# Optimization experiments

Hardware: AMD Instinct MI355X
Metric: run time of the kernel (lower is better)

Reference implementation:

```python
import jax, jax.numpy as jnp
import numpy as np

S, B, E, H, D, P = 4096, 8, 1024, 16, 64, 64


def setup_inputs() -> dict:
    key = jax.random.key(0)
    ks = jax.random.split(key, 6)
    scale = 1.0 / np.sqrt(E)
    return {
        "x": jax.random.normal(ks[0], (S, B, E), dtype=jnp.float32),
        "w_qkv": jax.random.normal(ks[1], (3 * E, E), dtype=jnp.float32) * scale,
        "w_out": jax.random.normal(ks[2], (E, E), dtype=jnp.float32) * scale,
        "b_out": jax.random.normal(ks[3], (E,), dtype=jnp.float32) * 0.01,
        "w_f": jax.random.normal(ks[4], (P, D), dtype=jnp.float32) * (1.0 / np.sqrt(D)),
        "b_f": jax.random.normal(ks[5], (P,), dtype=jnp.float32) * 0.01,
    }


def reference(x, w_qkv, w_out, b_out, w_f, b_f):
    # x: (S, B, E). qkv_proj has no bias.
    qkv = jnp.einsum("sbe,fe->sbf", x, w_qkv)  # (S, B, 3E)
    q, k, v = jnp.split(qkv, 3, axis=-1)

    def to_heads(t):
        # view (S,B,H,D) then transpose(0,2) -> (H,B,S,D)
        return t.reshape(S, B, H, D).transpose(2, 1, 0, 3)

    q, k, v = to_heads(q), to_heads(k), to_heads(v)

    # feature map: Linear(D->P) + ReLU, applied to q and k
    q_p = jax.nn.relu(jnp.einsum("hbsd,pd->hbsp", q, w_f) + b_f)
    k_p = jax.nn.relu(jnp.einsum("hbsd,pd->hbsp", k, w_f) + b_f)

    # linear attention: O(n) via k'^T v then q' @ (k'^T v)
    kv = jnp.einsum("hbsp,hbsd->hbpd", k_p, v)          # (H,B,P,D)
    num = jnp.einsum("hbsp,hbpd->hbsd", q_p, kv)         # (H,B,S,D)
    k_sum = k_p.sum(axis=-2)                              # (H,B,P)
    normalizer = jnp.einsum("hbsp,hbp->hbs", q_p, k_sum)[..., None]  # (H,B,S,1)
    attn = num / (normalizer + 1e-8)

    # back to (S, B, E)
    out = attn.transpose(2, 1, 0, 3).reshape(S, B, E)
    return jnp.einsum("sbe,fe->sbf", out, w_out) + b_out
```

## Files before the change

### kernel.cpp

```cpp
#include <hip/hip_runtime.h>
#include <hip/hip_bf16.h>
#include <stdint.h>

#define S_LEN 4096
#define B_DIM 8
#define E_DIM 1024
#define H_DIM 16
#define M_ROWS (S_LEN * B_DIM)
#define N_QKV (3 * E_DIM)
#define HB_DIM (H_DIM * B_DIM)

typedef float f32x4 __attribute__((ext_vector_type(4)));
typedef short bf16x8 __attribute__((ext_vector_type(8)));

#define MFMA16(a, b, c) __builtin_amdgcn_mfma_f32_16x16x32_bf16(a, b, c, 0, 0, 0)

__device__ __forceinline__ short f2bf(float f) {
  __hip_bfloat16 h = __float2bfloat16(f);
  short s;
  __builtin_memcpy(&s, &h, 2);
  return s;
}
__device__ __forceinline__ float bf2f(short b) {
  unsigned u = ((unsigned)(unsigned short)b) << 16;
  float f;
  __builtin_memcpy(&f, &u, 4);
  return f;
}
__device__ __forceinline__ void gl_lds16(const void* g, void* l) {
  __builtin_amdgcn_global_load_lds(
      (const __attribute__((address_space(1))) void*)g,
      (__attribute__((address_space(3))) void*)l, 16, 0, 0);
}

__global__ __launch_bounds__(256) void cast_all(
    const float* __restrict__ x, const float* __restrict__ wqkv,
    const float* __restrict__ wout, const float* __restrict__ wf,
    short* __restrict__ xb, short* __restrict__ wqb,
    short* __restrict__ wob, short* __restrict__ wfb) {
  const long n_x = (long)M_ROWS * E_DIM;
  const long n_wq = 3L * E_DIM * E_DIM;
  const long n_wo = (long)E_DIM * E_DIM;
  long idx = ((long)blockIdx.x * 256 + threadIdx.x) * 4;
  const float* src;
  short* dst;
  if (idx < n_x) {
    src = x + idx; dst = xb + idx;
  } else if ((idx -= n_x) < n_wq) {
    src = wqkv + idx; dst = wqb + idx;
  } else if ((idx -= n_wq) < n_wo) {
    src = wout + idx; dst = wob + idx;
  } else {
    idx -= n_wo;
    src = wf + idx; dst = wfb + idx;
  }
  float4 v = *(const float4*)src;
  short4 o;
  o.x = f2bf(v.x); o.y = f2bf(v.y); o.z = f2bf(v.z); o.w = f2bf(v.w);
  *(short4*)dst = o;
}

template <int OUT_F32>
__global__ __launch_bounds__(512, 2) void gemm256(
    const short* __restrict__ A, const short* __restrict__ Bm,
    void* __restrict__ Cout, const float* __restrict__ bias, int N, int K) {
  __shared__ short As[4 * 8192];
  __shared__ short Bs[4 * 8192];
  const int t = threadIdx.x;
  const int w = t >> 6, l = t & 63;
  const int q = l >> 4, c = l & 15;
  const int wm = w >> 2, wn = w & 3;

  const int nwg = gridDim.x;
  const int cpx = nwg >> 3;
  const int lid = ((int)blockIdx.x & 7) * cpx + ((int)blockIdx.x >> 3);
  const int bm = (lid & 127) << 8;
  const int bn = (lid >> 7) << 8;

  const long Kb = (long)K * 2;
  const int srow = t >> 2;
  const int scolb = (((t & 3) ^ ((t >> 3) & 3)) << 4);
  const char* gA = (const char*)A + (long)(bm + srow) * Kb + scolb;
  const char* gB = (const char*)Bm + (long)(bn + srow) * Kb + scolb;
  const long chb = 128 * Kb;
  char* lA = (char*)As + (w << 10);
  char* lB = (char*)Bs + (w << 10);

  const int qs = q ^ ((c >> 1) & 3);
  const short* ar = As + ((wm << 7) + c) * 32 + (qs << 3);
  const short* br = Bs + ((wn << 6) + c) * 32 + (qs << 3);

  f32x4 acc[8][4];
#pragma unroll
  for (int i = 0; i < 8; i++)
#pragma unroll
    for (int j = 0; j < 4; j++) acc[i][j] = (f32x4){0.f, 0.f, 0.f, 0.f};

#pragma unroll
  for (int p = 0; p < 3; p++) {
    const char* sa = gA + (long)p * 64;
    const char* sb = gB + (long)p * 64;
    char* da = lA + p * 16384;
    char* db = lB + p * 16384;
    gl_lds16(sa, da);
    gl_lds16(sa + chb, da + 8192);
    gl_lds16(sb, db);
    gl_lds16(sb + chb, db + 8192);
  }
  asm volatile("s_waitcnt vmcnt(8)\n\ts_barrier" ::: "memory");

  const int NT = K >> 5;
  for (int tt = 0; tt < NT; ++tt) {
    const int slot = (tt & 3) * 8192;
    const int pslot = ((tt + 3) & 3) * 16384;
    const int pkt = (tt + 3 < NT) ? tt + 3 : NT - 1;
    const short* ap = ar + slot;
    const short* bp = br + slot;
    const char* sa = gA + (long)pkt * 64;
    const char* sb = gB + (long)pkt * 64;

    bf16x8 af[8], bfr[4];
#pragma unroll
    for (int mi = 0; mi < 4; mi++) af[mi] = *(const bf16x8*)(ap + mi * 512);
#pragma unroll
    for (int ni = 0; ni < 4; ni++) bfr[ni] = *(const bf16x8*)(bp + ni * 512);
    gl_lds16(sa, lA + pslot);
    gl_lds16(sa + chb, lA + pslot + 8192);
    __builtin_amdgcn_s_barrier();
    __builtin_amdgcn_s_setprio(1);
#pragma unroll
    for (int mi = 0; mi < 4; mi++)
#pragma unroll
      for (int ni = 0; ni < 4; ni++)
        acc[mi][ni] = MFMA16(af[mi], bfr[ni], acc[mi][ni]);
    __builtin_amdgcn_s_setprio(0);
    __builtin_amdgcn_s_barrier();
#pragma unroll
    for (int mi = 4; mi < 8; mi++) af[mi] = *(const bf16x8*)(ap + mi * 512);
    gl_lds16(sb, lB + pslot);
    gl_lds16(sb + chb, lB + pslot + 8192);
    __builtin_amdgcn_s_barrier();
    __builtin_amdgcn_s_setprio(1);
#pragma unroll
    for (int mi = 4; mi < 8; mi++)
#pragma unroll
      for (int ni = 0; ni < 4; ni++)
        acc[mi][ni] = MFMA16(af[mi], bfr[ni], acc[mi][ni]);
    __builtin_amdgcn_s_setprio(0);
    asm volatile("s_waitcnt vmcnt(8)\n\ts_barrier" ::: "memory");
  }
  asm volatile("s_waitcnt vmcnt(0)" ::: "memory");

  if (OUT_F32) {
    float* C = (float*)Cout;
#pragma unroll
    for (int ni = 0; ni < 4; ni++) {
      int n = bn + (wn << 6) + ni * 16 + c;
      float bo = bias[n];
#pragma unroll
      for (int mi = 0; mi < 8; mi++)
#pragma unroll
        for (int r = 0; r < 4; r++) {
          int m = bm + (wm << 7) + mi * 16 + (q << 2) + r;
          C[(long)m * N + n] = acc[mi][ni][r] + bo;
        }
    }
  } else {
    short* C = (short*)Cout;
#pragma unroll
    for (int ni = 0; ni < 4; ni++) {
      int n = bn + (wn << 6) + ni * 16 + c;
#pragma unroll
      for (int mi = 0; mi < 8; mi++)
#pragma unroll
        for (int r = 0; r < 4; r++) {
          int m = bm + (wm << 7) + mi * 16 + (q << 2) + r;
          C[(long)m * N + n] = f2bf(acc[mi][ni][r]);
        }
    }
  }
}

__global__ __launch_bounds__(256) void feature_kernel(
    const short* __restrict__ qkv, const short* __restrict__ wfb,
    const float* __restrict__ b_f, short* __restrict__ Qp,
    short* __restrict__ KpT, short* __restrict__ VT) {
  const int bx = blockIdx.x;
  const int sblk = bx & 15, b = (bx >> 4) & 7, h = bx >> 7;
  const int t = threadIdx.x, w = t >> 6, l = t & 63;
  const int q = l >> 4, c = l & 15;
  const int s_base = sblk * 256 + w * 64;
  const int hb = h * 8 + b;

  bf16x8 wf[4][2];
#pragma unroll
  for (int ti = 0; ti < 4; ti++)
#pragma unroll
    for (int kk = 0; kk < 2; kk++)
      wf[ti][kk] = *(const bf16x8*)(wfb + (ti * 16 + c) * 64 + kk * 32 + q * 8);

  float bfc[4];
#pragma unroll
  for (int ni = 0; ni < 4; ni++) bfc[ni] = b_f[ni * 16 + c];

  f32x4 acc[4][4];
  bf16x8 xf[4][2];

#pragma unroll
  for (int i = 0; i < 4; i++)
#pragma unroll
    for (int j = 0; j < 4; j++) acc[i][j] = (f32x4){0.f, 0.f, 0.f, 0.f};
#pragma unroll
  for (int mi = 0; mi < 4; mi++) {
    long ridx = (long)((s_base + mi * 16 + c) * 8 + b) * N_QKV;
#pragma unroll
    for (int kk = 0; kk < 2; kk++)
      xf[mi][kk] = *(const bf16x8*)(qkv + ridx + h * 64 + kk * 32 + q * 8);
  }
#pragma unroll
  for (int kk = 0; kk < 2; kk++)
#pragma unroll
    for (int mi = 0; mi < 4; mi++)
#pragma unroll
      for (int ni = 0; ni < 4; ni++)
        acc[mi][ni] = MFMA16(xf[mi][kk], wf[ni][kk], acc[mi][ni]);
#pragma unroll
  for (int mi = 0; mi < 4; mi++)
#pragma unroll
    for (int ni = 0; ni < 4; ni++)
#pragma unroll
      for (int r = 0; r < 4; r++) {
        int s = s_base + mi * 16 + q * 4 + r;
        float v = acc[mi][ni][r] + bfc[ni];
        v = fmaxf(v, 0.f);
        Qp[((long)hb * S_LEN + s) * 64 + ni * 16 + c] = f2bf(v);
      }

#pragma unroll
  for (int i = 0; i < 4; i++)
#pragma unroll
    for (int j = 0; j < 4; j++) acc[i][j] = (f32x4){0.f, 0.f, 0.f, 0.f};
#pragma unroll
  for (int si = 0; si < 4; si++) {
    long ridx = (long)((s_base + si * 16 + c) * 8 + b) * N_QKV;
#pragma unroll
    for (int kk = 0; kk < 2; kk++)
      xf[si][kk] =
          *(const bf16x8*)(qkv + ridx + E_DIM + h * 64 + kk * 32 + q * 8);
  }
#pragma unroll
  for (int kk = 0; kk < 2; kk++)
#pragma unroll
    for (int pi = 0; pi < 4; pi++)
#pragma unroll
      for (int si = 0; si < 4; si++)
        acc[pi][si] = MFMA16(wf[pi][kk], xf[si][kk], acc[pi][si]);
#pragma unroll
  for (int pi = 0; pi < 4; pi++)
#pragma unroll
    for (int r = 0; r < 4; r++) {
      int p = pi * 16 + q * 4 + r;
      float bb = b_f[p];
#pragma unroll
      for (int si = 0; si < 4; si++) {
        int s = s_base + si * 16 + c;
        float v = acc[pi][si][r] + bb;
        v = fmaxf(v, 0.f);
        KpT[((long)hb * 64 + p) * S_LEN + s] = f2bf(v);
      }
    }

  bf16x8 id0 = {0, 0, 0, 0, 0, 0, 0, 0}, id1 = {0, 0, 0, 0, 0, 0, 0, 0};
#pragma unroll
  for (int j = 0; j < 8; j++) {
    int k = q * 8 + j;
    id0[j] = (short)((k == c) ? 0x3F80 : 0);
    id1[j] = (short)((k == c + 16) ? 0x3F80 : 0);
  }
#pragma unroll
  for (int i = 0; i < 4; i++)
#pragma unroll
    for (int j = 0; j < 4; j++) acc[i][j] = (f32x4){0.f, 0.f, 0.f, 0.f};
#pragma unroll
  for (int si = 0; si < 4; si++) {
    long ridx = (long)((s_base + si * 16 + c) * 8 + b) * N_QKV;
#pragma unroll
    for (int kc = 0; kc < 2; kc++)
      xf[si][kc] =
          *(const bf16x8*)(qkv + ridx + 2 * E_DIM + h * 64 + kc * 32 + q * 8);
  }
#pragma unroll
  for (int kc = 0; kc < 2; kc++)
#pragma unroll
    for (int si = 0; si < 4; si++) {
      acc[kc * 2 + 0][si] = MFMA16(id0, xf[si][kc], acc[kc * 2 + 0][si]);
      acc[kc * 2 + 1][si] = MFMA16(id1, xf[si][kc], acc[kc * 2 + 1][si]);
    }
#pragma unroll
  for (int dt = 0; dt < 4; dt++)
#pragma unroll
    for (int si = 0; si < 4; si++)
#pragma unroll
      for (int r = 0; r < 4; r++) {
        int d = (dt >> 1) * 32 + (dt & 1) * 16 + q * 4 + r;
        int s = s_base + si * 16 + c;
        VT[((long)hb * 64 + d) * S_LEN + s] = f2bf(acc[dt][si][r]);
      }
}

__global__ __launch_bounds__(256) void kv_kernel(const short* __restrict__ KpT,
                                                 const short* __restrict__ VT,
                                                 float* __restrict__ kvf) {
  const int hb = blockIdx.y, sc = blockIdx.x;
  const int t = threadIdx.x, w = t >> 6, l = t & 63;
  const int q = l >> 4, c = l & 15;
  const int s0 = sc * 512 + w * 128;
  const short* vb = VT + (long)hb * 64 * S_LEN;
  const short* kb = KpT + (long)hb * 64 * S_LEN;

  f32x4 acc[4][4];
#pragma unroll
  for (int i = 0; i < 4; i++)
#pragma unroll
    for (int j = 0; j < 4; j++) acc[i][j] = (f32x4){0.f, 0.f, 0.f, 0.f};

  for (int it = 0; it < 4; it++) {
    int so = s0 + it * 32 + q * 8;
    bf16x8 af[4], bfr[4];
#pragma unroll
    for (int di = 0; di < 4; di++)
      af[di] = *(const bf16x8*)(vb + (long)(di * 16 + c) * S_LEN + so);
#pragma unroll
    for (int pi = 0; pi < 4; pi++)
      bfr[pi] = *(const bf16x8*)(kb + (long)(pi * 16 + c) * S_LEN + so);
#pragma unroll
    for (int di = 0; di < 4; di++)
#pragma unroll
      for (int pi = 0; pi < 4; pi++)
        acc[di][pi] = MFMA16(af[di], bfr[pi], acc[di][pi]);
  }

  __shared__ float red[4][4096];
#pragma unroll
  for (int di = 0; di < 4; di++)
#pragma unroll
    for (int pi = 0; pi < 4; pi++)
#pragma unroll
      for (int r = 0; r < 4; r++)
        red[w][(di * 16 + q * 4 + r) * 64 + pi * 16 + c] = acc[di][pi][r];
  __syncthreads();
  float* dst = kvf + (long)hb * 4096;
  for (int i = 0; i < 16; i++) {
    int idx = i * 256 + t;
    float s = red[0][idx] + red[1][idx] + red[2][idx] + red[3][idx];
    atomicAdd(dst + idx, s);
  }
}

__global__ __launch_bounds__(256) void kv_cast(const float* __restrict__ kvf,
                                               short* __restrict__ kvb) {
  int i = blockIdx.x * 256 + threadIdx.x;
  kvb[i] = f2bf(kvf[i]);
}

__global__ __launch_bounds__(256) void ksum_kernel(const short* __restrict__ KpT,
                                                   short* __restrict__ ksum) {
  const int hb = blockIdx.x;
  const int t = threadIdx.x, w = t >> 6, l = t & 63;
  for (int pi = 0; pi < 16; pi++) {
    int p = w * 16 + pi;
    const short* row = KpT + ((long)hb * 64 + p) * S_LEN;
    float s = 0.f;
#pragma unroll
    for (int i = 0; i < 8; i++) {
      bf16x8 v = *(const bf16x8*)(row + i * 512 + l * 8);
#pragma unroll
      for (int j = 0; j < 8; j++) s += bf2f(v[j]);
    }
    for (int off = 32; off > 0; off >>= 1) s += __shfl_down(s, off, 64);
    if (l == 0) ksum[hb * 64 + p] = f2bf(s);
  }
}

__global__ __launch_bounds__(256) void attn_kernel(
    const short* __restrict__ Qp, const short* __restrict__ kvb,
    const short* __restrict__ ksum, short* __restrict__ attn) {
  const int bx = blockIdx.x;
  const int sblk = bx & 15, b = (bx >> 4) & 7, h = bx >> 7;
  const int t = threadIdx.x, w = t >> 6, l = t & 63;
  const int q = l >> 4, c = l & 15;
  const int s_base = sblk * 256 + w * 64;
  const int hb = h * 8 + b;

  bf16x8 bkv[4][2];
#pragma unroll
  for (int ni = 0; ni < 4; ni++)
#pragma unroll
    for (int kk = 0; kk < 2; kk++)
      bkv[ni][kk] = *(const bf16x8*)(kvb + (long)hb * 4096 +
                                     (ni * 16 + c) * 64 + kk * 32 + q * 8);
  bf16x8 bn[2];
  const bf16x8 zfrag = {0, 0, 0, 0, 0, 0, 0, 0};
#pragma unroll
  for (int kk = 0; kk < 2; kk++) {
    bf16x8 v = *(const bf16x8*)(ksum + hb * 64 + kk * 32 + q * 8);
    bn[kk] = (c == 0) ? v : zfrag;
  }

  bf16x8 af[4][2];
#pragma unroll
  for (int mi = 0; mi < 4; mi++)
#pragma unroll
    for (int kk = 0; kk < 2; kk++)
      af[mi][kk] = *(const bf16x8*)(Qp + ((long)hb * S_LEN + s_base + mi * 16 + c) * 64 +
                                    kk * 32 + q * 8);

  f32x4 acc[4][4], accn[4];
#pragma unroll
  for (int i = 0; i < 4; i++) {
    accn[i] = (f32x4){0.f, 0.f, 0.f, 0.f};
#pragma unroll
    for (int j = 0; j < 4; j++) acc[i][j] = (f32x4){0.f, 0.f, 0.f, 0.f};
  }
#pragma unroll
  for (int kk = 0; kk < 2; kk++)
#pragma unroll
    for (int mi = 0; mi < 4; mi++) {
      accn[mi] = MFMA16(af[mi][kk], bn[kk], accn[mi]);
#pragma unroll
      for (int ni = 0; ni < 4; ni++)
        acc[mi][ni] = MFMA16(af[mi][kk], bkv[ni][kk], acc[mi][ni]);
    }

#pragma unroll
  for (int mi = 0; mi < 4; mi++)
#pragma unroll
    for (int r = 0; r < 4; r++) {
      float nv = __shfl(accn[mi][r], l & 48, 64);
      float inv = 1.f / (nv + 1e-8f);
      int s = s_base + mi * 16 + q * 4 + r;
#pragma unroll
      for (int ni = 0; ni < 4; ni++) {
        float v = acc[mi][ni][r] * inv;
        attn[((long)s * 8 + b) * E_DIM + h * 64 + ni * 16 + c] = f2bf(v);
      }
    }
}

extern "C" void kernel_launch(void* const* d_in, const int* in_sizes, int n_in,
                              void* d_out, int out_size, void* d_ws,
                              size_t ws_size, hipStream_t stream) {
  const float* x = (const float*)d_in[0];
  const float* w_qkv = (const float*)d_in[1];
  const float* w_out = (const float*)d_in[2];
  const float* b_out = (const float*)d_in[3];
  const float* w_f = (const float*)d_in[4];
  const float* b_f = (const float*)d_in[5];

  char* ws = (char*)d_ws;
  constexpr size_t off_xb = 0;
  constexpr size_t off_wqb = 67108864;
  constexpr size_t off_wob = off_wqb + 6291456;
  constexpr size_t off_wfb = off_wob + 2097152;
  constexpr size_t off_qkv = off_wfb + 8192;
  constexpr size_t off_Qp = off_qkv + 201326592;
  constexpr size_t off_KpT = off_Qp + 67108864;
  constexpr size_t off_VT = off_KpT + 67108864;
  constexpr size_t off_kvf = off_VT + 67108864;
  constexpr size_t off_kvb = off_kvf + 2097152;
  constexpr size_t off_ksum = off_kvb + 1048576;

  short* xb = (short*)(ws + off_xb);
  short* wqb = (short*)(ws + off_wqb);
  short* wob = (short*)(ws + off_wob);
  short* wfb = (short*)(ws + off_wfb);
  short* qkv = (short*)(ws + off_qkv);
  short* Qp = (short*)(ws + off_Qp);
  short* KpT = (short*)(ws + off_KpT);
  short* VT = (short*)(ws + off_VT);
  float* kvf = (float*)(ws + off_kvf);
  short* kvb = (short*)(ws + off_kvb);
  short* ksum = (short*)(ws + off_ksum);
  short* attn = xb;

  cast_all<<<36868, 256, 0, stream>>>(x, w_qkv, w_out, w_f, xb, wqb, wob, wfb);

  gemm256<0><<<1536, 512, 0, stream>>>(xb, wqb, qkv, nullptr, N_QKV, E_DIM);

  feature_kernel<<<2048, 256, 0, stream>>>(qkv, wfb, b_f, Qp, KpT, VT);

  hipMemsetAsync(kvf, 0, (size_t)HB_DIM * 4096 * 4, stream);
  kv_kernel<<<dim3(8, HB_DIM), 256, 0, stream>>>(KpT, VT, kvf);
  kv_cast<<<2048, 256, 0, stream>>>(kvf, kvb);
  ksum_kernel<<<HB_DIM, 256, 0, stream>>>(KpT, ksum);

  attn_kernel<<<2048, 256, 0, stream>>>(Qp, kvb, ksum, attn);

  gemm256<1><<<512, 512, 0, stream>>>(attn, wob, (float*)d_out, b_out,
                                      E_DIM, E_DIM);
}
```

Baseline: 862.6 us.

## Restructure GEMM mainloop to 64-wide K tiles with staggered A/B double buffering

The 256x256 bf16 GEMM mainloop moves from four 32-wide K stages to two 64-wide K buffers. A is prefetched one tile ahead and B two tiles ahead, and each iteration is split into four MFMA quarter phases. The LDS layout changes to a 128-byte row swizzle with an 8-way XOR. The aim is to halve the per-K barrier and loop overhead and to interleave global-to-LDS copies more finely with MFMA work. The cost is more barriers per iteration, more B fragment registers held live, and harder-to-verify buffer reuse timing.

```diff
diff --git a/kernel.cpp b/kernel.cpp
--- a/kernel.cpp
+++ b/kernel.cpp
@@ -60,12 +60,23 @@
   *(short4*)dst = o;
 }
 
+__device__ __forceinline__ void mma16q(f32x4 acc[8][4], const bf16x8 afr[2][2],
+                                       const bf16x8 bfr[4][2], int m0) {
+#pragma unroll
+  for (int kk = 0; kk < 2; kk++)
+#pragma unroll
+    for (int ii = 0; ii < 2; ii++)
+#pragma unroll
+      for (int ni = 0; ni < 4; ni++)
+        acc[m0 + ii][ni] = MFMA16(afr[ii][kk], bfr[ni][kk], acc[m0 + ii][ni]);
+}
+
 template <int OUT_F32>
 __global__ __launch_bounds__(512, 2) void gemm256(
     const short* __restrict__ A, const short* __restrict__ Bm,
     void* __restrict__ Cout, const float* __restrict__ bias, int N, int K) {
-  __shared__ short As[4 * 8192];
-  __shared__ short Bs[4 * 8192];
+  __shared__ short L[65536];
+  char* Lb = (char*)L;
   const int t = threadIdx.x;
   const int w = t >> 6, l = t & 63;
   const int q = l >> 4, c = l & 15;
@@ -78,17 +89,37 @@
   const int bn = (lid >> 7) << 8;
 
   const long Kb = (long)K * 2;
-  const int srow = t >> 2;
-  const int scolb = (((t & 3) ^ ((t >> 3) & 3)) << 4);
-  const char* gA = (const char*)A + (long)(bm + srow) * Kb + scolb;
-  const char* gB = (const char*)Bm + (long)(bn + srow) * Kb + scolb;
-  const long chb = 128 * Kb;
-  char* lA = (char*)As + (w << 10);
-  char* lB = (char*)Bs + (w << 10);
-
-  const int qs = q ^ ((c >> 1) & 3);
-  const short* ar = As + ((wm << 7) + c) * 32 + (qs << 3);
-  const short* br = Bs + ((wn << 6) + c) * 32 + (qs << 3);
+  const int srow = t >> 3;
+  const int scb = (((t & 7) ^ ((t >> 3) & 7)) << 4);
+  const char* gA = (const char*)A + (long)(bm + srow) * Kb + scb;
+  const char* gB = (const char*)Bm + (long)(bn + srow) * Kb + scb;
+  const long r64 = 64 * Kb;
+
+#define STAGE_A(h, srcT, dbuf)                                      \
+  do {                                                              \
+    const char* s_ = gA + (long)(srcT) * 128 + (long)(h) * 2 * r64; \
+    char* d_ = Lb + (dbuf) * 32768 + (h) * 16384 + (w << 10);       \
+    gl_lds16(s_, d_);                                               \
+    gl_lds16(s_ + r64, d_ + 8192);                                  \
+  } while (0)
+#define STAGE_B(h, srcT, dbuf)                                      \
+  do {                                                              \
+    const char* s_ = gB + (long)(srcT) * 128 + (long)(h) * 2 * r64; \
+    char* d_ = Lb + 65536 + (dbuf) * 32768 + (h) * 16384 + (w << 10); \
+    gl_lds16(s_, d_);                                               \
+    gl_lds16(s_ + r64, d_ + 8192);                                  \
+  } while (0)
+
+  const int sw = c & 7;
+  const int s0 = (q ^ sw) << 3;
+  const int s1 = s0 ^ 32;
+  const int aoff = wm * 8192 + c * 64;
+  const int boff = 32768 + (wn >> 1) * 8192 + ((wn & 1) * 64 + c) * 64;
+
+#define LDA(dst, mi, kk) \
+  dst = *(const bf16x8*)(L + bufo + aoff + (mi) * 1024 + ((kk) ? s1 : s0))
+#define LDB(dst, ni, kk) \
+  dst = *(const bf16x8*)(L + bufo + boff + (ni) * 1024 + ((kk) ? s1 : s0))
 
   f32x4 acc[8][4];
 #pragma unroll
@@ -96,60 +127,72 @@
 #pragma unroll
     for (int j = 0; j < 4; j++) acc[i][j] = (f32x4){0.f, 0.f, 0.f, 0.f};
 
-#pragma unroll
-  for (int p = 0; p < 3; p++) {
-    const char* sa = gA + (long)p * 64;
-    const char* sb = gB + (long)p * 64;
-    char* da = lA + p * 16384;
-    char* db = lB + p * 16384;
-    gl_lds16(sa, da);
-    gl_lds16(sa + chb, da + 8192);
-    gl_lds16(sb, db);
-    gl_lds16(sb + chb, db + 8192);
-  }
-  asm volatile("s_waitcnt vmcnt(8)\n\ts_barrier" ::: "memory");
-
-  const int NT = K >> 5;
-  for (int tt = 0; tt < NT; ++tt) {
-    const int slot = (tt & 3) * 8192;
-    const int pslot = ((tt + 3) & 3) * 16384;
-    const int pkt = (tt + 3 < NT) ? tt + 3 : NT - 1;
-    const short* ap = ar + slot;
-    const short* bp = br + slot;
-    const char* sa = gA + (long)pkt * 64;
-    const char* sb = gB + (long)pkt * 64;
-
-    bf16x8 af[8], bfr[4];
-#pragma unroll
-    for (int mi = 0; mi < 4; mi++) af[mi] = *(const bf16x8*)(ap + mi * 512);
-#pragma unroll
-    for (int ni = 0; ni < 4; ni++) bfr[ni] = *(const bf16x8*)(bp + ni * 512);
-    gl_lds16(sa, lA + pslot);
-    gl_lds16(sa + chb, lA + pslot + 8192);
+  const int NT = K >> 6;
+
+  STAGE_A(0, 0, 0);
+  STAGE_A(1, 0, 0);
+  STAGE_B(0, 0, 0);
+  STAGE_B(1, 0, 0);
+  STAGE_B(0, 1, 1);
+  STAGE_B(1, 1, 1);
+  asm volatile("s_waitcnt vmcnt(4)\n\ts_barrier" ::: "memory");
+
+  for (int T = 0; T < NT; ++T) {
+    const int bufo = (T & 1) * 16384;
+    const int TA = (T + 1 < NT) ? T + 1 : NT - 1;
+    const int TB = (T + 2 < NT) ? T + 2 : NT - 1;
+    const int bufA = (T + 1) & 1;
+    const int bufB = T & 1;
+
+    bf16x8 bfr[4][2], afr[2][2];
+
+#pragma unroll
+    for (int ni = 0; ni < 4; ni++) {
+      LDB(bfr[ni][0], ni, 0);
+      LDB(bfr[ni][1], ni, 1);
+    }
+    LDA(afr[0][0], 0, 0); LDA(afr[0][1], 0, 1);
+    LDA(afr[1][0], 1, 0); LDA(afr[1][1], 1, 1);
+    STAGE_A(0, TA, bufA);
     __builtin_amdgcn_s_barrier();
     __builtin_amdgcn_s_setprio(1);
-#pragma unroll
-    for (int mi = 0; mi < 4; mi++)
-#pragma unroll
-      for (int ni = 0; ni < 4; ni++)
-        acc[mi][ni] = MFMA16(af[mi], bfr[ni], acc[mi][ni]);
+    mma16q(acc, afr, bfr, 0);
     __builtin_amdgcn_s_setprio(0);
     __builtin_amdgcn_s_barrier();
-#pragma unroll
-    for (int mi = 4; mi < 8; mi++) af[mi] = *(const bf16x8*)(ap + mi * 512);
-    gl_lds16(sb, lB + pslot);
-    gl_lds16(sb + chb, lB + pslot + 8192);
+
+    LDA(afr[0][0], 2, 0); LDA(afr[0][1], 2, 1);
+    LDA(afr[1][0], 3, 0); LDA(afr[1][1], 3, 1);
+    STAGE_A(1, TA, bufA);
     __builtin_amdgcn_s_barrier();
     __builtin_amdgcn_s_setprio(1);
-#pragma unroll
-    for (int mi = 4; mi < 8; mi++)
-#pragma unroll
-      for (int ni = 0; ni < 4; ni++)
-        acc[mi][ni] = MFMA16(af[mi], bfr[ni], acc[mi][ni]);
+    mma16q(acc, afr, bfr, 2);
     __builtin_amdgcn_s_setprio(0);
-    asm volatile("s_waitcnt vmcnt(8)\n\ts_barrier" ::: "memory");
+    __builtin_amdgcn_s_barrier();
+
+    LDA(afr[0][0], 4, 0); LDA(afr[0][1], 4, 1);
+    LDA(afr[1][0], 5, 0); LDA(afr[1][1], 5, 1);
+    STAGE_B(0, TB, bufB);
+    __builtin_amdgcn_s_barrier();
+    __builtin_amdgcn_s_setprio(1);
+    mma16q(acc, afr, bfr, 4);
+    __builtin_amdgcn_s_setprio(0);
+    __builtin_amdgcn_s_barrier();
+
+    LDA(afr[0][0], 6, 0); LDA(afr[0][1], 6, 1);
+    LDA(afr[1][0], 7, 0); LDA(afr[1][1], 7, 1);
+    STAGE_B(1, TB, bufB);
+    __builtin_amdgcn_s_barrier();
+    __builtin_amdgcn_s_setprio(1);
+    mma16q(acc, afr, bfr, 6);
+    __builtin_amdgcn_s_setprio(0);
+    asm volatile("s_waitcnt vmcnt(4)\n\ts_barrier" ::: "memory");
   }
   asm volatile("s_waitcnt vmcnt(0)" ::: "memory");
+
+#undef STAGE_A
+#undef STAGE_B
+#undef LDA
+#undef LDB
 
   if (OUT_F32) {
     float* C = (float*)Cout;
```

After: 736.4 us. 14.6% less time.
